# Kernel optimization log

Hardware: AMD Instinct MI355X
Metric: run time of the kernel (lower is better)

## Reference

```python
import jax, jax.numpy as jnp
import numpy as np
from jax import lax

NPOINT = 1024   # FPS centroids
NSAMPLE = 32    # neighbors per ball
RADIUS = 0.1    # ball-query radius (points live in unit cube)


def farthest_point_sample(pos, npoint):
    # pos: [B, N, 3] -> idx [B, npoint] int32
    B, N, _ = pos.shape

    def step(carry, _):
        min_d, far = carry                                   # [B,N], [B]
        centroid = jnp.take_along_axis(pos, far[:, None, None], axis=1)  # [B,1,3]
        d = jnp.sum((pos - centroid) ** 2, axis=-1)          # [B,N]
        min_d = jnp.minimum(min_d, d)
        nxt = jnp.argmax(min_d, axis=1).astype(jnp.int32)
        return (min_d, nxt), far

    init = (jnp.full((B, N), 1e10, pos.dtype), jnp.zeros((B,), jnp.int32))
    _, idx = lax.scan(step, init, None, length=npoint)
    return idx.T                                             # [B, npoint]


def ball_query(new_pos, pos, radius, k):
    # new_pos: [B,M,3], pos: [B,N,3] -> idx [B,M,k] int32
    d2 = (jnp.sum(new_pos ** 2, -1)[:, :, None]
          + jnp.sum(pos ** 2, -1)[:, None, :]
          - 2.0 * jnp.einsum('bmc,bnc->bmn', new_pos, pos))  # [B,M,N]
    neg = jnp.where(d2 <= radius * radius, -d2, -jnp.inf)
    vals, idx = lax.top_k(neg, k)                            # k nearest inside ball
    valid = vals > -jnp.inf
    idx = jnp.where(valid, idx, idx[..., :1])                # replicate first hit (centroid itself)
    return idx.astype(jnp.int32)


def setup_inputs() -> dict:
    key = jax.random.key(0)
    ks = jax.random.split(key, 6)
    B, N, C = 4, 16384, 1
    pos = jax.random.uniform(ks[0], (B, N, 3), dtype=jnp.float32)
    x = jax.random.normal(ks[1], (B, N, C), dtype=jnp.float32)
    c_in = 3 + C  # rel-xyz concat features
    W1 = jax.random.normal(ks[2], (c_in, 32), jnp.float32) * np.sqrt(2.0 / c_in)
    W2 = jax.random.normal(ks[3], (32, 32), jnp.float32) * np.sqrt(2.0 / 32)
    W3 = jax.random.normal(ks[4], (32, 32), jnp.float32) * np.sqrt(2.0 / 32)
    b1 = jnp.zeros((32,), jnp.float32)
    b2 = jnp.zeros((32,), jnp.float32)
    b3 = jnp.zeros((32,), jnp.float32)
    return {"pos": pos, "x": x, "W1": W1, "b1": b1, "W2": W2, "b2": b2, "W3": W3, "b3": b3}


def reference(pos, x, W1, b1, W2, b2, W3, b3):
    # PointNet++ set-abstraction: FPS -> ball query -> group -> shared MLP -> max-pool.
    fps_idx = farthest_point_sample(lax.stop_gradient(pos), NPOINT)       # [B,M]
    new_pos = jnp.take_along_axis(pos, fps_idx[..., None], axis=1)        # [B,M,3]
    idx = ball_query(lax.stop_gradient(new_pos), lax.stop_gradient(pos), RADIUS, NSAMPLE)  # [B,M,K]
    B, M, K = idx.shape
    flat = idx.reshape(B, M * K)
    gpos = jnp.take_along_axis(pos, flat[..., None], axis=1).reshape(B, M, K, 3)
    gx = jnp.take_along_axis(x, flat[..., None], axis=1).reshape(B, M, K, -1)
    rel = gpos - new_pos[:, :, None, :]                                   # local coords
    h = jnp.concatenate([rel, gx], axis=-1)                               # [B,M,K,4]
    h = jax.nn.relu(h @ W1 + b1)
    h = jax.nn.relu(h @ W2 + b2)
    h = jax.nn.relu(h @ W3 + b3)
    return jnp.max(h, axis=2)                                             # [B,M,32]
```

## Files before the change

kernel.cpp:

```cpp
#include <hip/hip_runtime.h>

#define NB 4
#define NPT 16384
#define NPOINT 1024
#define NSAMPLE 32

#define FPS_T 1024
#define FPS_PPT (NPT / FPS_T)
#define FPS_W (FPS_T / 64)

#define BQ_WAVES 4
#define CAP 896

__global__ __launch_bounds__(FPS_T) void fps_kernel(const float* __restrict__ pos,
                                                    float* __restrict__ new_pos) {
#pragma clang fp contract(off)
  const int b = blockIdx.x;
  const int tid = threadIdx.x;
  const int wid = tid >> 6;
  const int lane = tid & 63;
  const float* __restrict__ p = pos + (size_t)b * NPT * 3;

  float px[FPS_PPT], py[FPS_PPT], pz[FPS_PPT], md[FPS_PPT];
#pragma unroll
  for (int i = 0; i < FPS_PPT; ++i) {
    const int n = tid + i * FPS_T;
    px[i] = p[n * 3 + 0];
    py[i] = p[n * 3 + 1];
    pz[i] = p[n * 3 + 2];
    md[i] = 1e10f;
  }

  __shared__ unsigned long long red[2][FPS_W];

  float cx = p[0], cy = p[1], cz = p[2];

  for (int j = 0; j < NPOINT; ++j) {
    if (tid == 0) {
      float* q = new_pos + ((size_t)b * NPOINT + j) * 3;
      q[0] = cx;
      q[1] = cy;
      q[2] = cz;
    }
    unsigned long long best = 0ull;
#pragma unroll
    for (int i = 0; i < FPS_PPT; ++i) {
      const float dx = px[i] - cx;
      const float dy = py[i] - cy;
      const float dz = pz[i] - cz;
      const float d = (dx * dx + dy * dy) + dz * dz;
      const float m = fminf(md[i], d);
      md[i] = m;
      const unsigned long long key =
          ((unsigned long long)__float_as_uint(m) << 32) |
          (unsigned)(~(tid + i * FPS_T));
      best = best < key ? key : best;
    }
#pragma unroll
    for (int off = 32; off > 0; off >>= 1) {
      const unsigned long long o = __shfl_xor(best, off, 64);
      best = best < o ? o : best;
    }
    if (lane == 0) red[j & 1][wid] = best;
    __syncthreads();
    unsigned long long w = red[j & 1][0];
#pragma unroll
    for (int k = 1; k < FPS_W; ++k) {
      const unsigned long long o = red[j & 1][k];
      w = w < o ? o : w;
    }
    const int nf = (int)(~(unsigned)(w & 0xFFFFFFFFull));
    cx = p[nf * 3 + 0];
    cy = p[nf * 3 + 1];
    cz = p[nf * 3 + 2];
  }
}

__global__ __launch_bounds__(256) void bq_mlp_kernel(
    const float* __restrict__ pos, const float* __restrict__ x,
    const float* __restrict__ W1, const float* __restrict__ b1,
    const float* __restrict__ W2, const float* __restrict__ b2,
    const float* __restrict__ W3, const float* __restrict__ b3,
    const float* __restrict__ new_pos, float* __restrict__ out) {
#pragma clang fp contract(off)
  __shared__ __align__(16) float w1s[4 * 32];
  __shared__ __align__(16) float w2s[32 * 32];
  __shared__ __align__(16) float w3s[32 * 32];
  __shared__ float b1s[32], b2s[32], b3s[32];
  __shared__ unsigned long long list[BQ_WAVES][CAP];
  __shared__ int sel[BQ_WAVES][NSAMPLE];
  __shared__ unsigned cnt[BQ_WAVES];

  const int tid = threadIdx.x;
  const int wid = tid >> 6;
  const int lane = tid & 63;

  for (int i = tid; i < 128; i += 256) w1s[i] = W1[i];
  for (int i = tid; i < 1024; i += 256) {
    w2s[i] = W2[i];
    w3s[i] = W3[i];
  }
  if (tid < 32) {
    b1s[tid] = b1[tid];
    b2s[tid] = b2[tid];
    b3s[tid] = b3[tid];
  }
  if (lane == 0) cnt[wid] = 0u;
  __syncthreads();

  const int m_global = blockIdx.x * BQ_WAVES + wid;
  const int b = m_global >> 10;
  const float* __restrict__ p = pos + (size_t)b * NPT * 3;
  const float* __restrict__ xb = x + (size_t)b * NPT;

  const float cx = new_pos[(size_t)m_global * 3 + 0];
  const float cy = new_pos[(size_t)m_global * 3 + 1];
  const float cz = new_pos[(size_t)m_global * 3 + 2];
  const float snew = (cx * cx + cy * cy) + cz * cz;

  for (int n = lane; n < NPT; n += 64) {
    const float px_ = p[n * 3 + 0];
    const float py_ = p[n * 3 + 1];
    const float pz_ = p[n * 3 + 2];
    const float spos = (px_ * px_ + py_ * py_) + pz_ * pz_;
    const float dot = (cx * px_ + cy * py_) + cz * pz_;
    const float d2 = (snew + spos) - 2.0f * dot;
    if (d2 <= 0.01f) {
      const unsigned u = __float_as_uint(d2);
      const unsigned key = (u & 0x80000000u) ? ~u : (u | 0x80000000u);
      const unsigned li = atomicAdd(&cnt[wid], 1u);
      if (li < CAP)
        list[wid][li] = ((unsigned long long)key << 32) | (unsigned)n;
    }
  }
  __syncthreads();

  int c = (int)cnt[wid];
  if (c > CAP) c = CAP;
  const int nsel = c < NSAMPLE ? c : NSAMPLE;

  for (int i = lane; i < c; i += 64) {
    const unsigned long long ki = list[wid][i];
    int rank = 0;
    for (int jj = 0; jj < c; ++jj) rank += (list[wid][jj] < ki) ? 1 : 0;
    if (rank < NSAMPLE) sel[wid][rank] = (int)(unsigned)(ki & 0xFFFFFFFFull);
  }
  __syncthreads();

  const bool active = (lane < nsel);
  const int n = sel[wid][active ? lane : 0];

  const float gpx = p[n * 3 + 0];
  const float gpy = p[n * 3 + 1];
  const float gpz = p[n * 3 + 2];
  const float gxv = xb[n];

  const float h0 = gpx - cx, h1i = gpy - cy, h2i = gpz - cz, h3i = gxv;

  float h1[32];
#pragma unroll
  for (int o = 0; o < 32; ++o) {
    float a = b1s[o];
    a += h0 * w1s[0 * 32 + o];
    a += h1i * w1s[1 * 32 + o];
    a += h2i * w1s[2 * 32 + o];
    a += h3i * w1s[3 * 32 + o];
    h1[o] = fmaxf(a, 0.0f);
  }

  float acc[32];
#pragma unroll
  for (int o = 0; o < 32; ++o) acc[o] = b2s[o];
  for (int k = 0; k < 32; ++k) {
    const float hk = h1[k];
    const float4* row = (const float4*)&w2s[k * 32];
#pragma unroll
    for (int q = 0; q < 8; ++q) {
      const float4 ww = row[q];
      acc[4 * q + 0] += hk * ww.x;
      acc[4 * q + 1] += hk * ww.y;
      acc[4 * q + 2] += hk * ww.z;
      acc[4 * q + 3] += hk * ww.w;
    }
  }
#pragma unroll
  for (int o = 0; o < 32; ++o) h1[o] = fmaxf(acc[o], 0.0f);

#pragma unroll
  for (int o = 0; o < 32; ++o) acc[o] = b3s[o];
  for (int k = 0; k < 32; ++k) {
    const float hk = h1[k];
    const float4* row = (const float4*)&w3s[k * 32];
#pragma unroll
    for (int q = 0; q < 8; ++q) {
      const float4 ww = row[q];
      acc[4 * q + 0] += hk * ww.x;
      acc[4 * q + 1] += hk * ww.y;
      acc[4 * q + 2] += hk * ww.z;
      acc[4 * q + 3] += hk * ww.w;
    }
  }
#pragma unroll
  for (int o = 0; o < 32; ++o)
    acc[o] = active ? fmaxf(acc[o], 0.0f) : -INFINITY;

#pragma unroll
  for (int mask = 1; mask <= 16; mask <<= 1) {
#pragma unroll
    for (int o = 0; o < 32; ++o)
      acc[o] = fmaxf(acc[o], __shfl_xor(acc[o], mask, 64));
  }

  if (lane == 0) {
    float4* o4 = (float4*)(out + (size_t)m_global * 32);
#pragma unroll
    for (int q = 0; q < 8; ++q)
      o4[q] = make_float4(acc[4 * q + 0], acc[4 * q + 1], acc[4 * q + 2],
                          acc[4 * q + 3]);
  }
}

extern "C" void kernel_launch(void* const* d_in, const int* in_sizes, int n_in,
                              void* d_out, int out_size, void* d_ws,
                              size_t ws_size, hipStream_t stream) {
  const float* pos = (const float*)d_in[0];
  const float* x = (const float*)d_in[1];
  const float* W1 = (const float*)d_in[2];
  const float* b1 = (const float*)d_in[3];
  const float* W2 = (const float*)d_in[4];
  const float* b2 = (const float*)d_in[5];
  const float* W3 = (const float*)d_in[6];
  const float* b3 = (const float*)d_in[7];
  float* out = (float*)d_out;
  float* new_pos = (float*)d_ws;

  fps_kernel<<<NB, FPS_T, 0, stream>>>(pos, new_pos);
  bq_mlp_kernel<<<(NB * NPOINT) / BQ_WAVES, 256, 0, stream>>>(
      pos, x, W1, b1, W2, b2, W3, b3, new_pos, out);
}
```

Baseline: 2.061 ms.

## Shrink FPS block, use wave ballot argmax with LDS atomicMax, vectorize loads

FPS now runs 512 threads, each holding 32 contiguous points loaded as float4. The per-point 64-bit key compare becomes a float max tracked with its local index. The wave reduction is a float shuffle max plus a ballot to find the winning lane. The cross-wave reduction replaces the per-wave slots and serial scan with one LDS atomicMax into a rotating triple buffer. The ball-query scan reads four points per lane with float4 loads. These aim to cut the per-iteration sync and reduction latency of the serial FPS loop and the global load count, at the cost of more registers per thread and contended LDS atomics. Tie-breaking still picks the lowest index.

```diff
diff --git a/kernel.cpp b/kernel.cpp
--- a/kernel.cpp
+++ b/kernel.cpp
@@ -5,15 +5,14 @@
 #define NPOINT 1024
 #define NSAMPLE 32
 
-#define FPS_T 1024
+#define FPS_T 512
 #define FPS_PPT (NPT / FPS_T)
-#define FPS_W (FPS_T / 64)
 
 #define BQ_WAVES 4
 #define CAP 896
 
-__global__ __launch_bounds__(FPS_T) void fps_kernel(const float* __restrict__ pos,
-                                                    float* __restrict__ new_pos) {
+__global__ __launch_bounds__(FPS_T, 2) void fps_kernel(
+    const float* __restrict__ pos, float* __restrict__ new_pos) {
 #pragma clang fp contract(off)
   const int b = blockIdx.x;
   const int tid = threadIdx.x;
@@ -22,16 +21,26 @@
   const float* __restrict__ p = pos + (size_t)b * NPT * 3;
 
   float px[FPS_PPT], py[FPS_PPT], pz[FPS_PPT], md[FPS_PPT];
-#pragma unroll
-  for (int i = 0; i < FPS_PPT; ++i) {
-    const int n = tid + i * FPS_T;
-    px[i] = p[n * 3 + 0];
-    py[i] = p[n * 3 + 1];
-    pz[i] = p[n * 3 + 2];
-    md[i] = 1e10f;
-  }
-
-  __shared__ unsigned long long red[2][FPS_W];
+
+  {
+    const float4* pf4 = (const float4*)(p + (size_t)tid * (FPS_PPT * 3));
+#pragma unroll
+    for (int k = 0; k < FPS_PPT / 4; ++k) {
+      const float4 a = pf4[3 * k + 0];
+      const float4 bq = pf4[3 * k + 1];
+      const float4 c = pf4[3 * k + 2];
+      px[4 * k + 0] = a.x; py[4 * k + 0] = a.y; pz[4 * k + 0] = a.z;
+      px[4 * k + 1] = a.w; py[4 * k + 1] = bq.x; pz[4 * k + 1] = bq.y;
+      px[4 * k + 2] = bq.z; py[4 * k + 2] = bq.w; pz[4 * k + 2] = c.x;
+      px[4 * k + 3] = c.y; py[4 * k + 3] = c.z; pz[4 * k + 3] = c.w;
+    }
+#pragma unroll
+    for (int i = 0; i < FPS_PPT; ++i) md[i] = 1e10f;
+  }
+
+  __shared__ unsigned long long red[3];
+  if (tid < 3) red[tid] = 0ull;
+  __syncthreads();
 
   float cx = p[0], cy = p[1], cz = p[2];
 
@@ -42,7 +51,8 @@
       q[1] = cy;
       q[2] = cz;
     }
-    unsigned long long best = 0ull;
+    float bm = -1.0f;
+    int bi = 0;
 #pragma unroll
     for (int i = 0; i < FPS_PPT; ++i) {
       const float dx = px[i] - cx;
@@ -51,25 +61,29 @@
       const float d = (dx * dx + dy * dy) + dz * dz;
       const float m = fminf(md[i], d);
       md[i] = m;
+      if (m > bm) {
+        bm = m;
+        bi = i;
+      }
+    }
+    float wm = bm;
+#pragma unroll
+    for (int off = 1; off < 64; off <<= 1)
+      wm = fmaxf(wm, __shfl_xor(wm, off, 64));
+    const unsigned long long tied = __ballot(bm == wm);
+    const int wl = __ffsll((long long)tied) - 1;
+    const int wbi = __shfl(bi, wl, 64);
+    const int widx = ((wid << 6) + wl) * FPS_PPT + wbi;
+    if (lane == 0) {
       const unsigned long long key =
-          ((unsigned long long)__float_as_uint(m) << 32) |
-          (unsigned)(~(tid + i * FPS_T));
-      best = best < key ? key : best;
-    }
-#pragma unroll
-    for (int off = 32; off > 0; off >>= 1) {
-      const unsigned long long o = __shfl_xor(best, off, 64);
-      best = best < o ? o : best;
-    }
-    if (lane == 0) red[j & 1][wid] = best;
+          ((unsigned long long)__float_as_uint(wm) << 32) |
+          (unsigned)(~widx);
+      atomicMax(&red[j % 3], key);
+    }
     __syncthreads();
-    unsigned long long w = red[j & 1][0];
-#pragma unroll
-    for (int k = 1; k < FPS_W; ++k) {
-      const unsigned long long o = red[j & 1][k];
-      w = w < o ? o : w;
-    }
-    const int nf = (int)(~(unsigned)(w & 0xFFFFFFFFull));
+    const unsigned long long w = red[j % 3];
+    if (tid == 0) red[(j + 2) % 3] = 0ull;
+    const int nf = (int)(~(unsigned)w);
     cx = p[nf * 3 + 0];
     cy = p[nf * 3 + 1];
     cz = p[nf * 3 + 2];
@@ -118,19 +132,29 @@
   const float cz = new_pos[(size_t)m_global * 3 + 2];
   const float snew = (cx * cx + cy * cy) + cz * cz;
 
-  for (int n = lane; n < NPT; n += 64) {
-    const float px_ = p[n * 3 + 0];
-    const float py_ = p[n * 3 + 1];
-    const float pz_ = p[n * 3 + 2];
-    const float spos = (px_ * px_ + py_ * py_) + pz_ * pz_;
-    const float dot = (cx * px_ + cy * py_) + cz * pz_;
-    const float d2 = (snew + spos) - 2.0f * dot;
-    if (d2 <= 0.01f) {
-      const unsigned u = __float_as_uint(d2);
-      const unsigned key = (u & 0x80000000u) ? ~u : (u | 0x80000000u);
-      const unsigned li = atomicAdd(&cnt[wid], 1u);
-      if (li < CAP)
-        list[wid][li] = ((unsigned long long)key << 32) | (unsigned)n;
+  for (int it = 0; it < NPT / 256; ++it) {
+    const int n0 = it * 256 + lane * 4;
+    const float4* pf4 = (const float4*)(p + (size_t)n0 * 3);
+    const float4 a = pf4[0];
+    const float4 bq = pf4[1];
+    const float4 c = pf4[2];
+    float qx[4], qy[4], qz[4];
+    qx[0] = a.x;  qy[0] = a.y;  qz[0] = a.z;
+    qx[1] = a.w;  qy[1] = bq.x; qz[1] = bq.y;
+    qx[2] = bq.z; qy[2] = bq.w; qz[2] = c.x;
+    qx[3] = c.y;  qy[3] = c.z;  qz[3] = c.w;
+#pragma unroll
+    for (int t = 0; t < 4; ++t) {
+      const float spos = (qx[t] * qx[t] + qy[t] * qy[t]) + qz[t] * qz[t];
+      const float dot = (cx * qx[t] + cy * qy[t]) + cz * qz[t];
+      const float d2 = (snew + spos) - 2.0f * dot;
+      if (d2 <= 0.01f) {
+        const unsigned u = __float_as_uint(d2);
+        const unsigned key = (u & 0x80000000u) ? ~u : (u | 0x80000000u);
+        const unsigned li = atomicAdd(&cnt[wid], 1u);
+        if (li < CAP)
+          list[wid][li] = ((unsigned long long)key << 32) | (unsigned)(n0 + t);
+      }
     }
   }
   __syncthreads();
```

Result: faster. 1.906 ms (-7.5%).
